# Kernel tuning notes

Measured on AMD Instinct MI355X. Metric: run time of the kernel, lower is better.

The kernel has to match this reference:

```python
import jax, jax.numpy as jnp
import numpy as np

B, C, H, W, D = 8, 64, 16, 16, 8  # D = spectral channel dim ('channle')
CQ = C // 8


def setup_inputs() -> dict:
    key = jax.random.key(0)
    ks = jax.random.split(key, 8)
    return {
        "x": jax.random.normal(ks[0], (B, C, H, W, D), dtype=jnp.float32),
        "Wq": jax.random.normal(ks[1], (CQ, C), dtype=jnp.float32) * (1.0 / np.sqrt(C)),
        "bq": jax.random.normal(ks[2], (CQ,), dtype=jnp.float32) * 0.02,
        "Wk": jax.random.normal(ks[3], (CQ, C), dtype=jnp.float32) * (1.0 / np.sqrt(C)),
        "bk": jax.random.normal(ks[4], (CQ,), dtype=jnp.float32) * 0.02,
        "Wv": jax.random.normal(ks[5], (C, C), dtype=jnp.float32) * (1.0 / np.sqrt(C)),
        "bv": jax.random.normal(ks[6], (C,), dtype=jnp.float32) * 0.02,
        "gamma": jax.random.normal(ks[7], (1,), dtype=jnp.float32),
    }


def reference(x, Wq, bq, Wk, bk, Wv, bv, gamma):
    b, c, h, w, d = x.shape
    n = h * w * d
    xf = x.reshape(b, c, n)  # flatten spatial+spectral, matches torch .view
    # 1x1x1 convs are channel-wise linear maps
    q = jnp.einsum('oc,bcn->bno', Wq, xf) + bq  # [B, N, CQ]
    k = jnp.einsum('oc,bcn->bon', Wk, xf) + bk[:, None]  # [B, CQ, N]
    energy = jnp.einsum('bno,bom->bnm', q, k)  # [B, N, N]
    attn = jax.nn.softmax(energy, axis=-1)
    v = jnp.einsum('oc,bcn->bon', Wv, xf) + bv[:, None]  # [B, C, N]
    # out[b,c,i] = sum_j v[b,c,j] * attn[b,i,j]  (bmm with attention^T)
    out = jnp.einsum('bcj,bij->bci', v, attn)
    out = out.reshape(b, c, h, w, d)
    return gamma * out + x
```

## Files before the change

### kernel.cpp

```cpp
#include <hip/hip_runtime.h>
#include <math.h>


#define NB  8
#define NC  64
#define NN  2048
#define L2E 1.44269504088896340736f
#define MST 36

typedef float f32x4 __attribute__((ext_vector_type(4)));
typedef __bf16 bf16x8 __attribute__((ext_vector_type(8)));
typedef __bf16 bf16x2 __attribute__((ext_vector_type(2)));
typedef unsigned short ushort_t;
typedef unsigned short us4 __attribute__((ext_vector_type(4)));

__device__ __forceinline__ unsigned short f2bf(float f) {
    unsigned u = __float_as_uint(f);
    u += 0x7fffu + ((u >> 16) & 1u);
    return (unsigned short)(u >> 16);
}
__device__ __forceinline__ float bf2f(unsigned short h) {
    return __uint_as_float(((unsigned)h) << 16);
}
__device__ __forceinline__ unsigned packbf(float a, float b) {
    union { bf16x2 v; unsigned u; } t;
    t.v = (bf16x2){ (__bf16)a, (__bf16)b };
    return t.u;
}

__global__ __launch_bounds__(256) void qkv_kernel(
    const float* __restrict__ x,
    const float* __restrict__ Wq, const float* __restrict__ bq,
    const float* __restrict__ Wk, const float* __restrict__ bk,
    const float* __restrict__ Wv, const float* __restrict__ bv,
    ushort_t* __restrict__ Qws, ushort_t* __restrict__ Kws,
    ushort_t* __restrict__ Vws)
{
    __shared__ float sWg[64][20];
    __shared__ float sB[16];
    __shared__ float sX[64][64];

    const int tid = threadIdx.x;
    const unsigned blk = blockIdx.x;
    const int b = blk & 7;
    const unsigned rest = blk >> 3;
    const unsigned pc = rest / 5u;
    const int og = (int)(rest - pc * 5u);
    const int n0 = (int)pc * 64;
    const int obase = og * 16;

    for (int idx = tid; idx < 1024; idx += 256) {
        const int o = idx >> 6;
        const int c = idx & 63;
        const int oo = obase + o;
        float w;
        if (oo < 8)       w = Wq[oo * NC + c] * L2E;
        else if (oo < 16) w = Wk[(oo - 8) * NC + c];
        else              w = Wv[(oo - 16) * NC + c];
        sWg[c][o] = w;
    }
    if (tid < 16) {
        const int oo = obase + tid;
        float v;
        if (oo < 8)       v = bq[oo] * L2E;
        else if (oo < 16) v = bk[oo - 8];
        else              v = bv[oo - 16];
        sB[tid] = v;
    }
    {
        const float* xg = x + (size_t)b * NC * NN + n0;
        for (int idx = tid; idx < 4096; idx += 256) {
            const int c = idx >> 6, px = idx & 63;
            sX[c][px] = xg[(size_t)c * NN + px];
        }
    }
    __syncthreads();

    const int lanepx = tid & 63;
    const int wv = tid >> 6;

    f32x4 acc = { sB[wv*4+0], sB[wv*4+1], sB[wv*4+2], sB[wv*4+3] };
    #pragma unroll
    for (int ch = 0; ch < 64; ch++) {
        const float xv = sX[ch][lanepx];
        const f32x4 w = *(const f32x4*)&sWg[ch][wv * 4];
        acc[0] = fmaf(w[0], xv, acc[0]);
        acc[1] = fmaf(w[1], xv, acc[1]);
        acc[2] = fmaf(w[2], xv, acc[2]);
        acc[3] = fmaf(w[3], xv, acc[3]);
    }

    const int n = n0 + lanepx;
    const int t  = n >> 6;

    if (og == 0) {
        us4 hi, lo;
        #pragma unroll
        for (int e = 0; e < 4; e++) {
            const unsigned short h = f2bf(acc[e]);
            hi[e] = h;
            lo[e] = f2bf(acc[e] - bf2f(h));
        }
        if (wv < 2) {
            const size_t a = (size_t)b * 32768 + (size_t)(n >> 4) * 256
                           + (size_t)(n & 15) * 8 + wv * 4;
            *(us4*)(Qws + a)       = hi;
            *(us4*)(Qws + a + 128) = lo;
        } else {
            const int jl = n & 63;
            const int fK = ((jl >> 5) & 1) + 2 * ((jl >> 2) & 1);
            const int mK = ((jl >> 3) & 3) * 4 + (jl & 3);
            const size_t a = (size_t)b * 32768 + (size_t)t * 1024
                           + (size_t)fK * 256 + (size_t)mK * 8 + (wv - 2) * 4;
            *(us4*)(Kws + a)       = hi;
            *(us4*)(Kws + a + 128) = lo;
        }
    } else {
        const int jc = (n >> 5) & 1;
        const int gg = (n >> 3) & 3;
        const int e8 = n & 7;
        const int cb = og - 1;
        const size_t base = (size_t)b * 131072 + (size_t)t * 4096
                          + (size_t)jc * 2048 + (size_t)cb * 512
                          + (size_t)gg * 8 + e8;
        #pragma unroll
        for (int e = 0; e < 4; e++)
            Vws[base + (size_t)(wv * 4 + e) * 32] = f2bf(acc[e]);
    }
}

__global__ __launch_bounds__(512, 2) void attn_kernel(
    const ushort_t* __restrict__ Qg, const ushort_t* __restrict__ Kg,
    const ushort_t* __restrict__ Vg, const float* __restrict__ x,
    const float* __restrict__ gamma, float* __restrict__ out)
{
    __shared__ __align__(16) char smem[74752];
    float* sMacc = (float*)smem;
    float* sMl   = (float*)(smem + 73728);

    const int tid  = threadIdx.x;
    const int w    = tid >> 6;
    const int rg   = w >> 2;
    const int jq   = w & 3;
    const int lane = tid & 63;
    const int li   = lane & 15;
    const int g    = lane >> 4;
    const int b    = blockIdx.x & 7;
    const int rb   = blockIdx.x >> 3;
    const int i0   = rb * 64 + rg * 32;

    const ushort_t* Kb = Kg + (size_t)b * 32768;
    const ushort_t* Vb = Vg + (size_t)b * 131072;

    const int ib0 = rb * 4 + rg * 2;
    const bf16x8 qf0 = *(const bf16x8*)(Qg + (size_t)b * 32768 + (size_t)ib0 * 256
                                        + (size_t)(g & 1) * 128 + (size_t)li * 8);
    const bf16x8 qf1 = *(const bf16x8*)(Qg + (size_t)b * 32768 + (size_t)(ib0 + 1) * 256
                                        + (size_t)(g & 1) * 128 + (size_t)li * 8);

    float l0 = 0.f, l1 = 0.f;
    f32x4 acc0[4], acc1[4];
    #pragma unroll
    for (int cb = 0; cb < 4; cb++) {
        acc0[cb] = (f32x4){0.f,0.f,0.f,0.f};
        acc1[cb] = (f32x4){0.f,0.f,0.f,0.f};
    }
    const f32x4 zero4 = {0.f,0.f,0.f,0.f};

    const ushort_t* Kp = Kb + (size_t)(jq * 8) * 1024 + (size_t)(g >> 1) * 128 + (size_t)li * 8;
    const ushort_t* Vp = Vb + (size_t)(jq * 8) * 4096 + (size_t)li * 32 + (size_t)g * 8;

    bf16x8 kc[4];
    #pragma unroll
    for (int f = 0; f < 4; f++)
        kc[f] = *(const bf16x8*)(Kp + (size_t)f * 256);

    for (int t = 0; t < 8; ++t) {
        bf16x8 vc0[4];
        #pragma unroll
        for (int cb = 0; cb < 4; cb++)
            vc0[cb] = *(const bf16x8*)(Vp + (size_t)cb * 512);

        f32x4 e[4];
        __builtin_amdgcn_s_setprio(1);
        #pragma unroll
        for (int f = 0; f < 4; f++)
            e[f] = __builtin_amdgcn_mfma_f32_16x16x32_bf16(kc[f], qf0, zero4, 0, 0, 0);
        __builtin_amdgcn_s_setprio(0);

        unsigned pkA0[4], pkB0[4];
        {
            float ls = 0.f;
            #pragma unroll
            for (int f = 0; f < 4; f++) {
                const float p0 = __builtin_amdgcn_exp2f(e[f][0]);
                const float p1 = __builtin_amdgcn_exp2f(e[f][1]);
                const float p2 = __builtin_amdgcn_exp2f(e[f][2]);
                const float p3 = __builtin_amdgcn_exp2f(e[f][3]);
                pkA0[f] = packbf(p0, p1);
                pkB0[f] = packbf(p2, p3);
                ls += (p0 + p1) + (p2 + p3);
            }
            l0 += ls;
        }

        __builtin_amdgcn_s_setprio(1);
        #pragma unroll
        for (int f = 0; f < 4; f++)
            e[f] = __builtin_amdgcn_mfma_f32_16x16x32_bf16(kc[f], qf1, zero4, 0, 0, 0);
        __builtin_amdgcn_s_setprio(0);

        if (t < 7) {
            #pragma unroll
            for (int f = 0; f < 4; f++)
                kc[f] = *(const bf16x8*)(Kp + 1024 + (size_t)f * 256);
        }
        Kp += 1024;

        unsigned pkA1[4], pkB1[4];
        {
            float ls = 0.f;
            #pragma unroll
            for (int f = 0; f < 4; f++) {
                const float p0 = __builtin_amdgcn_exp2f(e[f][0]);
                const float p1 = __builtin_amdgcn_exp2f(e[f][1]);
                const float p2 = __builtin_amdgcn_exp2f(e[f][2]);
                const float p3 = __builtin_amdgcn_exp2f(e[f][3]);
                pkA1[f] = packbf(p0, p1);
                pkB1[f] = packbf(p2, p3);
                ls += (p0 + p1) + (p2 + p3);
            }
            l1 += ls;
        }

        bf16x8 vc1[4];
        #pragma unroll
        for (int cb = 0; cb < 4; cb++)
            vc1[cb] = *(const bf16x8*)(Vp + 2048 + (size_t)cb * 512);

        __builtin_amdgcn_s_setprio(1);
        {
            union { unsigned u[4]; bf16x8 v; } pf0, pf1;
            pf0.u[0] = pkA0[0]; pf0.u[1] = pkB0[0]; pf0.u[2] = pkA0[2]; pf0.u[3] = pkB0[2];
            pf1.u[0] = pkA1[0]; pf1.u[1] = pkB1[0]; pf1.u[2] = pkA1[2]; pf1.u[3] = pkB1[2];
            #pragma unroll
            for (int cb = 0; cb < 4; cb++) {
                acc0[cb] = __builtin_amdgcn_mfma_f32_16x16x32_bf16(vc0[cb], pf0.v, acc0[cb], 0, 0, 0);
                acc1[cb] = __builtin_amdgcn_mfma_f32_16x16x32_bf16(vc0[cb], pf1.v, acc1[cb], 0, 0, 0);
            }
        }
        {
            union { unsigned u[4]; bf16x8 v; } pf0, pf1;
            pf0.u[0] = pkA0[1]; pf0.u[1] = pkB0[1]; pf0.u[2] = pkA0[3]; pf0.u[3] = pkB0[3];
            pf1.u[0] = pkA1[1]; pf1.u[1] = pkB1[1]; pf1.u[2] = pkA1[3]; pf1.u[3] = pkB1[3];
            #pragma unroll
            for (int cb = 0; cb < 4; cb++) {
                acc0[cb] = __builtin_amdgcn_mfma_f32_16x16x32_bf16(vc1[cb], pf0.v, acc0[cb], 0, 0, 0);
                acc1[cb] = __builtin_amdgcn_mfma_f32_16x16x32_bf16(vc1[cb], pf1.v, acc1[cb], 0, 0, 0);
            }
        }
        __builtin_amdgcn_s_setprio(0);
        Vp += 4096;
    }

    l0 += __shfl_xor(l0, 16); l0 += __shfl_xor(l0, 32);
    l1 += __shfl_xor(l1, 16); l1 += __shfl_xor(l1, 32);

    __syncthreads();
    {
        float* ap = sMacc + (size_t)(w * 64 + lane) * MST;
        #pragma unroll
        for (int cb = 0; cb < 4; cb++) {
            *(f32x4*)(ap + cb * 4)      = acc0[cb];
            *(f32x4*)(ap + 16 + cb * 4) = acc1[cb];
        }
        if (g == 0) {
            sMl[w * 32 + li]      = l0;
            sMl[w * 32 + 16 + li] = l1;
        }
    }
    __syncthreads();

    {
        const int r = lane & 31;
        const float gmv = gamma[0];
        #pragma unroll
        for (int u = 0; u < 2; u++) {
            const int cq   = jq * 4 + (lane >> 5) * 2 + u;
            const int g_s  = cq & 3;
            const int cb_s = cq >> 2;
            const int ib_s = r >> 4;
            const int li_s = r & 15;
            const int srcln = g_s * 16 + li_s;
            const int aidx  = ib_s * 16 + cb_s * 4;

            float L = 0.f;
            float num0 = 0.f, num1 = 0.f, num2 = 0.f, num3 = 0.f;
            #pragma unroll
            for (int q = 0; q < 4; q++) {
                const int w2 = rg * 4 + q;
                L += sMl[w2 * 32 + r];
                const f32x4 a = *(const f32x4*)(sMacc + (size_t)(w2 * 64 + srcln) * MST + aidx);
                num0 += a[0]; num1 += a[1]; num2 += a[2]; num3 += a[3];
            }
            const float inv = 1.0f / L;
            const size_t gb = (size_t)b * NC * NN + i0 + r;
            const size_t c0 = (size_t)cq * 4;
            out[gb + (c0 + 0) * NN] = fmaf(gmv, num0 * inv, x[gb + (c0 + 0) * NN]);
            out[gb + (c0 + 1) * NN] = fmaf(gmv, num1 * inv, x[gb + (c0 + 1) * NN]);
            out[gb + (c0 + 2) * NN] = fmaf(gmv, num2 * inv, x[gb + (c0 + 2) * NN]);
            out[gb + (c0 + 3) * NN] = fmaf(gmv, num3 * inv, x[gb + (c0 + 3) * NN]);
        }
    }
}

extern "C" void kernel_launch(void* const* d_in, const int* in_sizes, int n_in,
                              void* d_out, int out_size, void* d_ws, size_t ws_size,
                              hipStream_t stream) {
    const float* x     = (const float*)d_in[0];
    const float* Wq    = (const float*)d_in[1];
    const float* bq    = (const float*)d_in[2];
    const float* Wk    = (const float*)d_in[3];
    const float* bk    = (const float*)d_in[4];
    const float* Wv    = (const float*)d_in[5];
    const float* bv    = (const float*)d_in[6];
    const float* gamma = (const float*)d_in[7];
    float* out = (float*)d_out;

    ushort_t* Qws = (ushort_t*)d_ws;
    ushort_t* Kws = Qws + (size_t)NB * 32768;
    ushort_t* Vws = Kws + (size_t)NB * 32768;

    qkv_kernel<<<1280, 256, 0, stream>>>(x, Wq, bq, Wk, bk, Wv, bv, Qws, Kws, Vws);
    attn_kernel<<<NB * 32, 512, 0, stream>>>(Qws, Kws, Vws, x, gamma, out);
}
```

Measured before the change: 24.20 us.

## Software-pipeline attention loop so PV MFMAs overlap next QK and exp

Restructures the inner loop into a software pipeline. A prologue computes the first tile's scores and probabilities. Each later iteration issues the next QK MFMAs together with the PV MFMAs of the previous tile, prefetches V one full tile ahead, and then runs the exp/pack work, with an epilogue finishing the last PV. The aim is to hide exp latency and global V load latency behind MFMA work, at the cost of more live registers (double-buffered V, 16 packed probability words) and a fully unrolled loop, which may hurt occupancy.

```diff
diff --git a/kernel.cpp b/kernel.cpp
--- a/kernel.cpp
+++ b/kernel.cpp
@@ -167,100 +167,136 @@
     }
     const f32x4 zero4 = {0.f,0.f,0.f,0.f};
 
-    const ushort_t* Kp = Kb + (size_t)(jq * 8) * 1024 + (size_t)(g >> 1) * 128 + (size_t)li * 8;
-    const ushort_t* Vp = Vb + (size_t)(jq * 8) * 4096 + (size_t)li * 32 + (size_t)g * 8;
-
-    bf16x8 kc[4];
-    #pragma unroll
-    for (int f = 0; f < 4; f++)
-        kc[f] = *(const bf16x8*)(Kp + (size_t)f * 256);
-
-    for (int t = 0; t < 8; ++t) {
-        bf16x8 vc0[4];
-        #pragma unroll
-        for (int cb = 0; cb < 4; cb++)
-            vc0[cb] = *(const bf16x8*)(Vp + (size_t)cb * 512);
-
-        f32x4 e[4];
+    const ushort_t* Kq = Kb + (size_t)(jq * 8) * 1024 + (size_t)(g >> 1) * 128 + (size_t)li * 8;
+    const ushort_t* Vq = Vb + (size_t)(jq * 8) * 4096 + (size_t)li * 32 + (size_t)g * 8;
+
+    bf16x8 kc[4], vcA[8];
+    unsigned pkP[16];
+
+    #pragma unroll
+    for (int f = 0; f < 4; f++) kc[f] = *(const bf16x8*)(Kq + (size_t)f * 256);
+    #pragma unroll
+    for (int u = 0; u < 8; u++)
+        vcA[u] = *(const bf16x8*)(Vq + (size_t)(u >> 2) * 2048 + (size_t)(u & 3) * 512);
+
+    {
+        f32x4 e0[4], e1[4];
         __builtin_amdgcn_s_setprio(1);
         #pragma unroll
         for (int f = 0; f < 4; f++)
-            e[f] = __builtin_amdgcn_mfma_f32_16x16x32_bf16(kc[f], qf0, zero4, 0, 0, 0);
+            e0[f] = __builtin_amdgcn_mfma_f32_16x16x32_bf16(kc[f], qf0, zero4, 0, 0, 0);
+        #pragma unroll
+        for (int f = 0; f < 4; f++)
+            e1[f] = __builtin_amdgcn_mfma_f32_16x16x32_bf16(kc[f], qf1, zero4, 0, 0, 0);
         __builtin_amdgcn_s_setprio(0);
-
-        unsigned pkA0[4], pkB0[4];
+        #pragma unroll
+        for (int f = 0; f < 4; f++)
+            kc[f] = *(const bf16x8*)(Kq + 1024 + (size_t)f * 256);
+        float ls0 = 0.f, ls1 = 0.f;
+        #pragma unroll
+        for (int f = 0; f < 4; f++) {
+            const float a0 = __builtin_amdgcn_exp2f(e0[f][0]);
+            const float a1 = __builtin_amdgcn_exp2f(e0[f][1]);
+            const float a2 = __builtin_amdgcn_exp2f(e0[f][2]);
+            const float a3 = __builtin_amdgcn_exp2f(e0[f][3]);
+            pkP[f]     = packbf(a0, a1);
+            pkP[4 + f] = packbf(a2, a3);
+            ls0 += (a0 + a1) + (a2 + a3);
+            const float c0 = __builtin_amdgcn_exp2f(e1[f][0]);
+            const float c1 = __builtin_amdgcn_exp2f(e1[f][1]);
+            const float c2 = __builtin_amdgcn_exp2f(e1[f][2]);
+            const float c3 = __builtin_amdgcn_exp2f(e1[f][3]);
+            pkP[8 + f]  = packbf(c0, c1);
+            pkP[12 + f] = packbf(c2, c3);
+            ls1 += (c0 + c1) + (c2 + c3);
+        }
+        l0 += ls0; l1 += ls1;
+    }
+
+    #pragma unroll
+    for (int t = 0; t < 7; ++t) {
+        bf16x8 vcB[8];
+        #pragma unroll
+        for (int u = 0; u < 8; u++)
+            vcB[u] = *(const bf16x8*)(Vq + (size_t)(t + 1) * 4096
+                                      + (size_t)(u >> 2) * 2048 + (size_t)(u & 3) * 512);
+
+        f32x4 e0[4], e1[4];
+        __builtin_amdgcn_s_setprio(1);
+        #pragma unroll
+        for (int f = 0; f < 4; f++)
+            e0[f] = __builtin_amdgcn_mfma_f32_16x16x32_bf16(kc[f], qf0, zero4, 0, 0, 0);
+        #pragma unroll
+        for (int f = 0; f < 4; f++)
+            e1[f] = __builtin_amdgcn_mfma_f32_16x16x32_bf16(kc[f], qf1, zero4, 0, 0, 0);
+
         {
-            float ls = 0.f;
+            union { unsigned u[4]; bf16x8 v; } pf0, pf1;
+            pf0.u[0] = pkP[0]; pf0.u[1] = pkP[4]; pf0.u[2] = pkP[2]; pf0.u[3] = pkP[6];
+            pf1.u[0] = pkP[8]; pf1.u[1] = pkP[12]; pf1.u[2] = pkP[10]; pf1.u[3] = pkP[14];
             #pragma unroll
-            for (int f = 0; f < 4; f++) {
-                const float p0 = __builtin_amdgcn_exp2f(e[f][0]);
-                const float p1 = __builtin_amdgcn_exp2f(e[f][1]);
-                const float p2 = __builtin_amdgcn_exp2f(e[f][2]);
-                const float p3 = __builtin_amdgcn_exp2f(e[f][3]);
-                pkA0[f] = packbf(p0, p1);
-                pkB0[f] = packbf(p2, p3);
-                ls += (p0 + p1) + (p2 + p3);
+            for (int cb = 0; cb < 4; cb++) {
+                acc0[cb] = __builtin_amdgcn_mfma_f32_16x16x32_bf16(vcA[cb], pf0.v, acc0[cb], 0, 0, 0);
+                acc1[cb] = __builtin_amdgcn_mfma_f32_16x16x32_bf16(vcA[cb], pf1.v, acc1[cb], 0, 0, 0);
             }
-            l0 += ls;
-        }
-
-        __builtin_amdgcn_s_setprio(1);
-        #pragma unroll
-        for (int f = 0; f < 4; f++)
-            e[f] = __builtin_amdgcn_mfma_f32_16x16x32_bf16(kc[f], qf1, zero4, 0, 0, 0);
+            pf0.u[0] = pkP[1]; pf0.u[1] = pkP[5]; pf0.u[2] = pkP[3]; pf0.u[3] = pkP[7];
+            pf1.u[0] = pkP[9]; pf1.u[1] = pkP[13]; pf1.u[2] = pkP[11]; pf1.u[3] = pkP[15];
+            #pragma unroll
+            for (int cb = 0; cb < 4; cb++) {
+                acc0[cb] = __builtin_amdgcn_mfma_f32_16x16x32_bf16(vcA[4 + cb], pf0.v, acc0[cb], 0, 0, 0);
+                acc1[cb] = __builtin_amdgcn_mfma_f32_16x16x32_bf16(vcA[4 + cb], pf1.v, acc1[cb], 0, 0, 0);
+            }
+        }
         __builtin_amdgcn_s_setprio(0);
 
-        if (t < 7) {
+        if (t < 6) {
             #pragma unroll
             for (int f = 0; f < 4; f++)
-                kc[f] = *(const bf16x8*)(Kp + 1024 + (size_t)f * 256);
-        }
-        Kp += 1024;
-
-        unsigned pkA1[4], pkB1[4];
-        {
-            float ls = 0.f;
-            #pragma unroll
-            for (int f = 0; f < 4; f++) {
-                const float p0 = __builtin_amdgcn_exp2f(e[f][0]);
-                const float p1 = __builtin_amdgcn_exp2f(e[f][1]);
-                const float p2 = __builtin_amdgcn_exp2f(e[f][2]);
-                const float p3 = __builtin_amdgcn_exp2f(e[f][3]);
-                pkA1[f] = packbf(p0, p1);
-                pkB1[f] = packbf(p2, p3);
-                ls += (p0 + p1) + (p2 + p3);
-            }
-            l1 += ls;
-        }
-
-        bf16x8 vc1[4];
-        #pragma unroll
-        for (int cb = 0; cb < 4; cb++)
-            vc1[cb] = *(const bf16x8*)(Vp + 2048 + (size_t)cb * 512);
-
+                kc[f] = *(const bf16x8*)(Kq + (size_t)(t + 2) * 1024 + (size_t)f * 256);
+        }
+
+        float ls0 = 0.f, ls1 = 0.f;
+        #pragma unroll
+        for (int f = 0; f < 4; f++) {
+            const float a0 = __builtin_amdgcn_exp2f(e0[f][0]);
+            const float a1 = __builtin_amdgcn_exp2f(e0[f][1]);
+            const float a2 = __builtin_amdgcn_exp2f(e0[f][2]);
+            const float a3 = __builtin_amdgcn_exp2f(e0[f][3]);
+            pkP[f]     = packbf(a0, a1);
+            pkP[4 + f] = packbf(a2, a3);
+            ls0 += (a0 + a1) + (a2 + a3);
+            const float c0 = __builtin_amdgcn_exp2f(e1[f][0]);
+            const float c1 = __builtin_amdgcn_exp2f(e1[f][1]);
+            const float c2 = __builtin_amdgcn_exp2f(e1[f][2]);
+            const float c3 = __builtin_amdgcn_exp2f(e1[f][3]);
+            pkP[8 + f]  = packbf(c0, c1);
+            pkP[12 + f] = packbf(c2, c3);
+            ls1 += (c0 + c1) + (c2 + c3);
+        }
+        l0 += ls0; l1 += ls1;
+
+        #pragma unroll
+        for (int u = 0; u < 8; u++) vcA[u] = vcB[u];
+    }
+
+    {
+        union { unsigned u[4]; bf16x8 v; } pf0, pf1;
         __builtin_amdgcn_s_setprio(1);
-        {
-            union { unsigned u[4]; bf16x8 v; } pf0, pf1;
-            pf0.u[0] = pkA0[0]; pf0.u[1] = pkB0[0]; pf0.u[2] = pkA0[2]; pf0.u[3] = pkB0[2];
-            pf1.u[0] = pkA1[0]; pf1.u[1] = pkB1[0]; pf1.u[2] = pkA1[2]; pf1.u[3] = pkB1[2];
-            #pragma unroll
-            for (int cb = 0; cb < 4; cb++) {
-                acc0[cb] = __builtin_amdgcn_mfma_f32_16x16x32_bf16(vc0[cb], pf0.v, acc0[cb], 0, 0, 0);
-                acc1[cb] = __builtin_amdgcn_mfma_f32_16x16x32_bf16(vc0[cb], pf1.v, acc1[cb], 0, 0, 0);
-            }
-        }
-        {
-            union { unsigned u[4]; bf16x8 v; } pf0, pf1;
-            pf0.u[0] = pkA0[1]; pf0.u[1] = pkB0[1]; pf0.u[2] = pkA0[3]; pf0.u[3] = pkB0[3];
-            pf1.u[0] = pkA1[1]; pf1.u[1] = pkB1[1]; pf1.u[2] = pkA1[3]; pf1.u[3] = pkB1[3];
-            #pragma unroll
-            for (int cb = 0; cb < 4; cb++) {
-                acc0[cb] = __builtin_amdgcn_mfma_f32_16x16x32_bf16(vc1[cb], pf0.v, acc0[cb], 0, 0, 0);
-                acc1[cb] = __builtin_amdgcn_mfma_f32_16x16x32_bf16(vc1[cb], pf1.v, acc1[cb], 0, 0, 0);
-            }
+        pf0.u[0] = pkP[0]; pf0.u[1] = pkP[4]; pf0.u[2] = pkP[2]; pf0.u[3] = pkP[6];
+        pf1.u[0] = pkP[8]; pf1.u[1] = pkP[12]; pf1.u[2] = pkP[10]; pf1.u[3] = pkP[14];
+        #pragma unroll
+        for (int cb = 0; cb < 4; cb++) {
+            acc0[cb] = __builtin_amdgcn_mfma_f32_16x16x32_bf16(vcA[cb], pf0.v, acc0[cb], 0, 0, 0);
+            acc1[cb] = __builtin_amdgcn_mfma_f32_16x16x32_bf16(vcA[cb], pf1.v, acc1[cb], 0, 0, 0);
+        }
+        pf0.u[0] = pkP[1]; pf0.u[1] = pkP[5]; pf0.u[2] = pkP[3]; pf0.u[3] = pkP[7];
+        pf1.u[0] = pkP[9]; pf1.u[1] = pkP[13]; pf1.u[2] = pkP[11]; pf1.u[3] = pkP[15];
+        #pragma unroll
+        for (int cb = 0; cb < 4; cb++) {
+            acc0[cb] = __builtin_amdgcn_mfma_f32_16x16x32_bf16(vcA[4 + cb], pf0.v, acc0[cb], 0, 0, 0);
+            acc1[cb] = __builtin_amdgcn_mfma_f32_16x16x32_bf16(vcA[4 + cb], pf1.v, acc1[cb], 0, 0, 0);
         }
         __builtin_amdgcn_s_setprio(0);
-        Vp += 4096;
     }
 
     l0 += __shfl_xor(l0, 16); l0 += __shfl_xor(l0, 32);
```

After: 24.45 us. Within noise of the previous version (+1.0%).

## Fuse QKV projection and attention into one kernel with a grid-wide flag barrier

Applied to the files above, without the earlier changes.

Merges the QKV projection kernel and the attention kernel into a single persistent launch of 256 blocks. Each block first projects its 64-pixel tile to all 80 output channels and writes Q/K/V to the workspace. A global atomic counter, reset by a memset before the launch, then acts as a grid barrier before the attention phase. This removes one kernel launch and the gap between the two kernels. In exchange the projection now runs on only 256 blocks instead of 1280, and correctness relies on all 256 blocks being resident at once.

```diff
diff --git a/kernel.cpp b/kernel.cpp
--- a/kernel.cpp
+++ b/kernel.cpp
@@ -7,6 +7,7 @@
 #define NN  2048
 #define L2E 1.44269504088896340736f
 #define MST 36
+#define FLAG_OFF 3145728
 
 typedef float f32x4 __attribute__((ext_vector_type(4)));
 typedef __bf16 bf16x8 __attribute__((ext_vector_type(8)));
@@ -28,288 +29,317 @@
     return t.u;
 }
 
-__global__ __launch_bounds__(256) void qkv_kernel(
+__global__ __launch_bounds__(512, 2) void pam_fused(
     const float* __restrict__ x,
     const float* __restrict__ Wq, const float* __restrict__ bq,
     const float* __restrict__ Wk, const float* __restrict__ bk,
     const float* __restrict__ Wv, const float* __restrict__ bv,
+    const float* __restrict__ gamma,
     ushort_t* __restrict__ Qws, ushort_t* __restrict__ Kws,
-    ushort_t* __restrict__ Vws)
+    ushort_t* __restrict__ Vws, unsigned* __restrict__ flag,
+    float* __restrict__ out)
 {
-    __shared__ float sWg[64][20];
-    __shared__ float sB[16];
-    __shared__ float sX[64][64];
+    __shared__ __align__(16) char smem[74752];
 
     const int tid = threadIdx.x;
-    const unsigned blk = blockIdx.x;
-    const int b = blk & 7;
-    const unsigned rest = blk >> 3;
-    const unsigned pc = rest / 5u;
-    const int og = (int)(rest - pc * 5u);
-    const int n0 = (int)pc * 64;
-    const int obase = og * 16;
-
-    for (int idx = tid; idx < 1024; idx += 256) {
-        const int o = idx >> 6;
-        const int c = idx & 63;
-        const int oo = obase + o;
-        float w;
-        if (oo < 8)       w = Wq[oo * NC + c] * L2E;
-        else if (oo < 16) w = Wk[(oo - 8) * NC + c];
-        else              w = Wv[(oo - 16) * NC + c];
-        sWg[c][o] = w;
+    const int b  = blockIdx.x & 7;
+    const int rb = blockIdx.x >> 3;
+
+    {
+        float* sW = (float*)smem;
+        float* sX = (float*)smem + 6400;
+        float* sB = (float*)smem + 6400 + 4352;
+
+        for (int idx = tid; idx < 5120; idx += 512) {
+            const int o = idx >> 6, c = idx & 63;
+            float w;
+            if (o < 8)       w = Wq[o * NC + c] * L2E;
+            else if (o < 16) w = Wk[(o - 8) * NC + c];
+            else             w = Wv[(o - 16) * NC + c];
+            sW[c * 100 + (o / 10) * 12 + (o % 10)] = w;
+        }
+        if (tid < 80) {
+            const int o = tid;
+            float v;
+            if (o < 8)       v = bq[o] * L2E;
+            else if (o < 16) v = bk[o - 8];
+            else             v = bv[o - 16];
+            sB[(o / 10) * 12 + (o % 10)] = v;
+        }
+        {
+            const float* xg = x + (size_t)b * NC * NN + rb * 64;
+            for (int idx = tid; idx < 4096; idx += 512) {
+                const int c = idx >> 6, px = idx & 63;
+                sX[c * 68 + px] = xg[(size_t)c * NN + px];
+            }
+        }
+        __syncthreads();
+
+        const int px = tid & 63;
+        const int sg = tid >> 6;
+        const int n  = rb * 64 + px;
+
+        f32x4 a0 = *(const f32x4*)(sB + sg * 12);
+        f32x4 a1 = *(const f32x4*)(sB + sg * 12 + 4);
+        f32x4 a2 = *(const f32x4*)(sB + sg * 12 + 8);
+        const float* wrow = sW + sg * 12;
+        #pragma unroll
+        for (int ch = 0; ch < 64; ch++) {
+            const float xv = sX[ch * 68 + px];
+            const f32x4 w0 = *(const f32x4*)(wrow + ch * 100);
+            const f32x4 w1 = *(const f32x4*)(wrow + ch * 100 + 4);
+            const f32x4 w2 = *(const f32x4*)(wrow + ch * 100 + 8);
+            a0[0] = fmaf(w0[0], xv, a0[0]); a0[1] = fmaf(w0[1], xv, a0[1]);
+            a0[2] = fmaf(w0[2], xv, a0[2]); a0[3] = fmaf(w0[3], xv, a0[3]);
+            a1[0] = fmaf(w1[0], xv, a1[0]); a1[1] = fmaf(w1[1], xv, a1[1]);
+            a1[2] = fmaf(w1[2], xv, a1[2]); a1[3] = fmaf(w1[3], xv, a1[3]);
+            a2[0] = fmaf(w2[0], xv, a2[0]); a2[1] = fmaf(w2[1], xv, a2[1]);
+            a2[2] = fmaf(w2[2], xv, a2[2]); a2[3] = fmaf(w2[3], xv, a2[3]);
+        }
+
+        float av[10];
+        av[0]=a0[0]; av[1]=a0[1]; av[2]=a0[2]; av[3]=a0[3];
+        av[4]=a1[0]; av[5]=a1[1]; av[6]=a1[2]; av[7]=a1[3];
+        av[8]=a2[0]; av[9]=a2[1];
+
+        const int jl = px;
+        const int fK = ((jl >> 5) & 1) + 2 * ((jl >> 2) & 1);
+        const int mK = ((jl >> 3) & 3) * 4 + (jl & 3);
+        const size_t kbase = (size_t)b * 32768 + (size_t)rb * 1024
+                           + (size_t)fK * 256 + (size_t)mK * 8;
+        const int jc = (px >> 5) & 1;
+        const int gg = (px >> 3) & 3;
+        const int e8 = px & 7;
+        const size_t vbase = (size_t)b * 131072 + (size_t)rb * 4096
+                           + (size_t)jc * 2048 + (size_t)gg * 8 + e8;
+
+        if (sg == 0) {
+            us4 h0, h1, l0v, l1v;
+            #pragma unroll
+            for (int e = 0; e < 4; e++) {
+                const unsigned short h = f2bf(av[e]);
+                h0[e] = h; l0v[e] = f2bf(av[e] - bf2f(h));
+            }
+            #pragma unroll
+            for (int e = 0; e < 4; e++) {
+                const unsigned short h = f2bf(av[4 + e]);
+                h1[e] = h; l1v[e] = f2bf(av[4 + e] - bf2f(h));
+            }
+            const size_t qa = (size_t)b * 32768 + (size_t)(n >> 4) * 256
+                            + (size_t)(n & 15) * 8;
+            *(us4*)(Qws + qa)       = h0; *(us4*)(Qws + qa + 4)       = h1;
+            *(us4*)(Qws + qa + 128) = l0v; *(us4*)(Qws + qa + 132)    = l1v;
+            #pragma unroll
+            for (int u = 8; u < 10; u++) {
+                const unsigned short h = f2bf(av[u]);
+                Kws[kbase + (u - 8)]       = h;
+                Kws[kbase + (u - 8) + 128] = f2bf(av[u] - bf2f(h));
+            }
+        } else if (sg == 1) {
+            #pragma unroll
+            for (int u = 0; u < 6; u++) {
+                const unsigned short h = f2bf(av[u]);
+                Kws[kbase + 2 + u]       = h;
+                Kws[kbase + 2 + u + 128] = f2bf(av[u] - bf2f(h));
+            }
+            #pragma unroll
+            for (int u = 6; u < 10; u++) {
+                const int c = u - 6;
+                Vws[vbase + (size_t)(c >> 4) * 512 + (size_t)(c & 15) * 32] = f2bf(av[u]);
+            }
+        } else {
+            #pragma unroll
+            for (int u = 0; u < 10; u++) {
+                const int c = sg * 10 - 16 + u;
+                Vws[vbase + (size_t)(c >> 4) * 512 + (size_t)(c & 15) * 32] = f2bf(av[u]);
+            }
+        }
     }
-    if (tid < 16) {
-        const int oo = obase + tid;
-        float v;
-        if (oo < 8)       v = bq[oo] * L2E;
-        else if (oo < 16) v = bk[oo - 8];
-        else              v = bv[oo - 16];
-        sB[tid] = v;
-    }
-    {
-        const float* xg = x + (size_t)b * NC * NN + n0;
-        for (int idx = tid; idx < 4096; idx += 256) {
-            const int c = idx >> 6, px = idx & 63;
-            sX[c][px] = xg[(size_t)c * NN + px];
-        }
+
+    __syncthreads();
+    __threadfence();
+    if (tid == 0) {
+        __hip_atomic_fetch_add(flag, 1u, __ATOMIC_ACQ_REL, __HIP_MEMORY_SCOPE_AGENT);
+        while (__hip_atomic_load(flag, __ATOMIC_ACQUIRE, __HIP_MEMORY_SCOPE_AGENT) < 256u)
+            __builtin_amdgcn_s_sleep(8);
     }
     __syncthreads();
-
-    const int lanepx = tid & 63;
-    const int wv = tid >> 6;
-
-    f32x4 acc = { sB[wv*4+0], sB[wv*4+1], sB[wv*4+2], sB[wv*4+3] };
-    #pragma unroll
-    for (int ch = 0; ch < 64; ch++) {
-        const float xv = sX[ch][lanepx];
-        const f32x4 w = *(const f32x4*)&sWg[ch][wv * 4];
-        acc[0] = fmaf(w[0], xv, acc[0]);
-        acc[1] = fmaf(w[1], xv, acc[1]);
-        acc[2] = fmaf(w[2], xv, acc[2]);
-        acc[3] = fmaf(w[3], xv, acc[3]);
-    }
-
-    const int n = n0 + lanepx;
-    const int t  = n >> 6;
-
-    if (og == 0) {
-        us4 hi, lo;
+    __threadfence();
+
+    {
+        float* sMacc = (float*)smem;
+        float* sMl   = (float*)(smem + 73728);
+
+        const int w    = tid >> 6;
+        const int rg   = w >> 2;
+        const int jq   = w & 3;
+        const int lane = tid & 63;
+        const int li   = lane & 15;
+        const int g    = lane >> 4;
+        const int i0   = rb * 64 + rg * 32;
+
+        const ushort_t* Kb = Kws + (size_t)b * 32768;
+        const ushort_t* Vb = Vws + (size_t)b * 131072;
+
+        const int ib0 = rb * 4 + rg * 2;
+        const bf16x8 qf0 = *(const bf16x8*)(Qws + (size_t)b * 32768 + (size_t)ib0 * 256
+                                            + (size_t)(g & 1) * 128 + (size_t)li * 8);
+        const bf16x8 qf1 = *(const bf16x8*)(Qws + (size_t)b * 32768 + (size_t)(ib0 + 1) * 256
+                                            + (size_t)(g & 1) * 128 + (size_t)li * 8);
+
+        float l0 = 0.f, l1 = 0.f;
+        f32x4 acc0[4], acc1[4];
         #pragma unroll
-        for (int e = 0; e < 4; e++) {
-            const unsigned short h = f2bf(acc[e]);
-            hi[e] = h;
-            lo[e] = f2bf(acc[e] - bf2f(h));
-        }
-        if (wv < 2) {
-            const size_t a = (size_t)b * 32768 + (size_t)(n >> 4) * 256
-                           + (size_t)(n & 15) * 8 + wv * 4;
-            *(us4*)(Qws + a)       = hi;
-            *(us4*)(Qws + a + 128) = lo;
-        } else {
-            const int jl = n & 63;
-            const int fK = ((jl >> 5) & 1) + 2 * ((jl >> 2) & 1);
-            const int mK = ((jl >> 3) & 3) * 4 + (jl & 3);
-            const size_t a = (size_t)b * 32768 + (size_t)t * 1024
-                           + (size_t)fK * 256 + (size_t)mK * 8 + (wv - 2) * 4;
-            *(us4*)(Kws + a)       = hi;
-            *(us4*)(Kws + a + 128) = lo;
-        }
-    } else {
-        const int jc = (n >> 5) & 1;
-        const int gg = (n >> 3) & 3;
-        const int e8 = n & 7;
-        const int cb = og - 1;
-        const size_t base = (size_t)b * 131072 + (size_t)t * 4096
-                          + (size_t)jc * 2048 + (size_t)cb * 512
-                          + (size_t)gg * 8 + e8;
-        #pragma unroll
-        for (int e = 0; e < 4; e++)
-            Vws[base + (size_t)(wv * 4 + e) * 32] = f2bf(acc[e]);
-    }
-}
-
-__global__ __launch_bounds__(512, 2) void attn_kernel(
-    const ushort_t* __restrict__ Qg, const ushort_t* __restrict__ Kg,
-    const ushort_t* __restrict__ Vg, const float* __restrict__ x,
-    const float* __restrict__ gamma, float* __restrict__ out)
-{
-    __shared__ __align__(16) char smem[74752];
-    float* sMacc = (float*)smem;
-    float* sMl   = (float*)(smem + 73728);
-
-    const int tid  = threadIdx.x;
-    const int w    = tid >> 6;
-    const int rg   = w >> 2;
-    const int jq   = w & 3;
-    const int lane = tid & 63;
-    const int li   = lane & 15;
-    const int g    = lane >> 4;
-    const int b    = blockIdx.x & 7;
-    const int rb   = blockIdx.x >> 3;
-    const int i0   = rb * 64 + rg * 32;
-
-    const ushort_t* Kb = Kg + (size_t)b * 32768;
-    const ushort_t* Vb = Vg + (size_t)b * 131072;
-
-    const int ib0 = rb * 4 + rg * 2;
-    const bf16x8 qf0 = *(const bf16x8*)(Qg + (size_t)b * 32768 + (size_t)ib0 * 256
-                                        + (size_t)(g & 1) * 128 + (size_t)li * 8);
-    const bf16x8 qf1 = *(const bf16x8*)(Qg + (size_t)b * 32768 + (size_t)(ib0 + 1) * 256
-                                        + (size_t)(g & 1) * 128 + (size_t)li * 8);
-
-    float l0 = 0.f, l1 = 0.f;
-    f32x4 acc0[4], acc1[4];
-    #pragma unroll
-    for (int cb = 0; cb < 4; cb++) {
-        acc0[cb] = (f32x4){0.f,0.f,0.f,0.f};
-        acc1[cb] = (f32x4){0.f,0.f,0.f,0.f};
-    }
-    const f32x4 zero4 = {0.f,0.f,0.f,0.f};
-
-    const ushort_t* Kp = Kb + (size_t)(jq * 8) * 1024 + (size_t)(g >> 1) * 128 + (size_t)li * 8;
-    const ushort_t* Vp = Vb + (size_t)(jq * 8) * 4096 + (size_t)li * 32 + (size_t)g * 8;
-
-    bf16x8 kc[4];
-    #pragma unroll
-    for (int f = 0; f < 4; f++)
-        kc[f] = *(const bf16x8*)(Kp + (size_t)f * 256);
-
-    for (int t = 0; t < 8; ++t) {
-        bf16x8 vc0[4];
-        #pragma unroll
-        for (int cb = 0; cb < 4; cb++)
-            vc0[cb] = *(const bf16x8*)(Vp + (size_t)cb * 512);
-
-        f32x4 e[4];
-        __builtin_amdgcn_s_setprio(1);
+        for (int cb = 0; cb < 4; cb++) {
+            acc0[cb] = (f32x4){0.f,0.f,0.f,0.f};
+            acc1[cb] = (f32x4){0.f,0.f,0.f,0.f};
+        }
+        const f32x4 zero4 = {0.f,0.f,0.f,0.f};
+
+        const ushort_t* Kp = Kb + (size_t)(jq * 8) * 1024 + (size_t)(g >> 1) * 128 + (size_t)li * 8;
+        const ushort_t* Vp = Vb + (size_t)(jq * 8) * 4096 + (size_t)li * 32 + (size_t)g * 8;
+
+        bf16x8 kc[4];
         #pragma unroll
         for (int f = 0; f < 4; f++)
-            e[f] = __builtin_amdgcn_mfma_f32_16x16x32_bf16(kc[f], qf0, zero4, 0, 0, 0);
-        __builtin_amdgcn_s_setprio(0);
-
-        unsigned pkA0[4], pkB0[4];
+            kc[f] = *(const bf16x8*)(Kp + (size_t)f * 256);
+
+        for (int t = 0; t < 8; ++t) {
+            bf16x8 vc0[4];
+            #pragma unroll
+            for (int cb = 0; cb < 4; cb++)
+                vc0[cb] = *(const bf16x8*)(Vp + (size_t)cb * 512);
+
+            f32x4 e[4];
+            __builtin_amdgcn_s_setprio(1);
+            #pragma unroll
+            for (int f = 0; f < 4; f++)
+                e[f] = __builtin_amdgcn_mfma_f32_16x16x32_bf16(kc[f], qf0, zero4, 0, 0, 0);
+            __builtin_amdgcn_s_setprio(0);
+
+            unsigned pkA0[4], pkB0[4];
+            {
+                float ls = 0.f;
+                #pragma unroll
+                for (int f = 0; f < 4; f++) {
+                    const float p0 = __builtin_amdgcn_exp2f(e[f][0]);
+                    const float p1 = __builtin_amdgcn_exp2f(e[f][1]);
+                    const float p2 = __builtin_amdgcn_exp2f(e[f][2]);
+                    const float p3 = __builtin_amdgcn_exp2f(e[f][3]);
+                    pkA0[f] = packbf(p0, p1);
+                    pkB0[f] = packbf(p2, p3);
+                    ls += (p0 + p1) + (p2 + p3);
+                }
+                l0 += ls;
+            }
+
+            __builtin_amdgcn_s_setprio(1);
+            #pragma unroll
+            for (int f = 0; f < 4; f++)
+                e[f] = __builtin_amdgcn_mfma_f32_16x16x32_bf16(kc[f], qf1, zero4, 0, 0, 0);
+            __builtin_amdgcn_s_setprio(0);
+
+            if (t < 7) {
+                #pragma unroll
+                for (int f = 0; f < 4; f++)
+                    kc[f] = *(const bf16x8*)(Kp + 1024 + (size_t)f * 256);
+            }
+            Kp += 1024;
+
+            unsigned pkA1[4], pkB1[4];
+            {
+                float ls = 0.f;
+                #pragma unroll
+                for (int f = 0; f < 4; f++) {
+                    const float p0 = __builtin_amdgcn_exp2f(e[f][0]);
+                    const float p1 = __builtin_amdgcn_exp2f(e[f][1]);
+                    const float p2 = __builtin_amdgcn_exp2f(e[f][2]);
+                    const float p3 = __builtin_amdgcn_exp2f(e[f][3]);
+                    pkA1[f] = packbf(p0, p1);
+                    pkB1[f] = packbf(p2, p3);
+                    ls += (p0 + p1) + (p2 + p3);
+                }
+                l1 += ls;
+            }
+
+            bf16x8 vc1[4];
+            #pragma unroll
+            for (int cb = 0; cb < 4; cb++)
+                vc1[cb] = *(const bf16x8*)(Vp + 2048 + (size_t)cb * 512);
+
+            __builtin_amdgcn_s_setprio(1);
+            {
+                union { unsigned u[4]; bf16x8 v; } pf0, pf1;
+                pf0.u[0] = pkA0[0]; pf0.u[1] = pkB0[0]; pf0.u[2] = pkA0[2]; pf0.u[3] = pkB0[2];
+                pf1.u[0] = pkA1[0]; pf1.u[1] = pkB1[0]; pf1.u[2] = pkA1[2]; pf1.u[3] = pkB1[2];
+                #pragma unroll
+                for (int cb = 0; cb < 4; cb++) {
+                    acc0[cb] = __builtin_amdgcn_mfma_f32_16x16x32_bf16(vc0[cb], pf0.v, acc0[cb], 0, 0, 0);
+                    acc1[cb] = __builtin_amdgcn_mfma_f32_16x16x32_bf16(vc0[cb], pf1.v, acc1[cb], 0, 0, 0);
+                }
+            }
+            {
+                union { unsigned u[4]; bf16x8 v; } pf0, pf1;
+                pf0.u[0] = pkA0[1]; pf0.u[1] = pkB0[1]; pf0.u[2] = pkA0[3]; pf0.u[3] = pkB0[3];
+                pf1.u[0] = pkA1[1]; pf1.u[1] = pkB1[1]; pf1.u[2] = pkA1[3]; pf1.u[3] = pkB1[3];
+                #pragma unroll
+                for (int cb = 0; cb < 4; cb++) {
+                    acc0[cb] = __builtin_amdgcn_mfma_f32_16x16x32_bf16(vc1[cb], pf0.v, acc0[cb], 0, 0, 0);
+                    acc1[cb] = __builtin_amdgcn_mfma_f32_16x16x32_bf16(vc1[cb], pf1.v, acc1[cb], 0, 0, 0);
+                }
+            }
+            __builtin_amdgcn_s_setprio(0);
+            Vp += 4096;
+        }
+
+        l0 += __shfl_xor(l0, 16); l0 += __shfl_xor(l0, 32);
+        l1 += __shfl_xor(l1, 16); l1 += __shfl_xor(l1, 32);
+
+        __syncthreads();
         {
-            float ls = 0.f;
-            #pragma unroll
-            for (int f = 0; f < 4; f++) {
-                const float p0 = __builtin_amdgcn_exp2f(e[f][0]);
-                const float p1 = __builtin_amdgcn_exp2f(e[f][1]);
-                const float p2 = __builtin_amdgcn_exp2f(e[f][2]);
-                const float p3 = __builtin_amdgcn_exp2f(e[f][3]);
-                pkA0[f] = packbf(p0, p1);
-                pkB0[f] = packbf(p2, p3);
-                ls += (p0 + p1) + (p2 + p3);
-            }
-            l0 += ls;
-        }
-
-        __builtin_amdgcn_s_setprio(1);
-        #pragma unroll
-        for (int f = 0; f < 4; f++)
-            e[f] = __builtin_amdgcn_mfma_f32_16x16x32_bf16(kc[f], qf1, zero4, 0, 0, 0);
-        __builtin_amdgcn_s_setprio(0);
-
-        if (t < 7) {
-            #pragma unroll
-            for (int f = 0; f < 4; f++)
-                kc[f] = *(const bf16x8*)(Kp + 1024 + (size_t)f * 256);
-        }
-        Kp += 1024;
-
-        unsigned pkA1[4], pkB1[4];
+            float* ap = sMacc + (size_t)(w * 64 + lane) * MST;
+            #pragma unroll
+            for (int cb = 0; cb < 4; cb++) {
+                *(f32x4*)(ap + cb * 4)      = acc0[cb];
+                *(f32x4*)(ap + 16 + cb * 4) = acc1[cb];
+            }
+            if (g == 0) {
+                sMl[w * 32 + li]      = l0;
+                sMl[w * 32 + 16 + li] = l1;
+            }
+        }
+        __syncthreads();
+
         {
-            float ls = 0.f;
-            #pragma unroll
-            for (int f = 0; f < 4; f++) {
-                const float p0 = __builtin_amdgcn_exp2f(e[f][0]);
-                const float p1 = __builtin_amdgcn_exp2f(e[f][1]);
-                const float p2 = __builtin_amdgcn_exp2f(e[f][2]);
-                const float p3 = __builtin_amdgcn_exp2f(e[f][3]);
-                pkA1[f] = packbf(p0, p1);
-                pkB1[f] = packbf(p2, p3);
-                ls += (p0 + p1) + (p2 + p3);
-            }
-            l1 += ls;
-        }
-
-        bf16x8 vc1[4];
-        #pragma unroll
-        for (int cb = 0; cb < 4; cb++)
-            vc1[cb] = *(const bf16x8*)(Vp + 2048 + (size_t)cb * 512);
-
-        __builtin_amdgcn_s_setprio(1);
-        {
-            union { unsigned u[4]; bf16x8 v; } pf0, pf1;
-            pf0.u[0] = pkA0[0]; pf0.u[1] = pkB0[0]; pf0.u[2] = pkA0[2]; pf0.u[3] = pkB0[2];
-            pf1.u[0] = pkA1[0]; pf1.u[1] = pkB1[0]; pf1.u[2] = pkA1[2]; pf1.u[3] = pkB1[2];
-            #pragma unroll
-            for (int cb = 0; cb < 4; cb++) {
-                acc0[cb] = __builtin_amdgcn_mfma_f32_16x16x32_bf16(vc0[cb], pf0.v, acc0[cb], 0, 0, 0);
-                acc1[cb] = __builtin_amdgcn_mfma_f32_16x16x32_bf16(vc0[cb], pf1.v, acc1[cb], 0, 0, 0);
-            }
-        }
-        {
-            union { unsigned u[4]; bf16x8 v; } pf0, pf1;
-            pf0.u[0] = pkA0[1]; pf0.u[1] = pkB0[1]; pf0.u[2] = pkA0[3]; pf0.u[3] = pkB0[3];
-            pf1.u[0] = pkA1[1]; pf1.u[1] = pkB1[1]; pf1.u[2] = pkA1[3]; pf1.u[3] = pkB1[3];
-            #pragma unroll
-            for (int cb = 0; cb < 4; cb++) {
-                acc0[cb] = __builtin_amdgcn_mfma_f32_16x16x32_bf16(vc1[cb], pf0.v, acc0[cb], 0, 0, 0);
-                acc1[cb] = __builtin_amdgcn_mfma_f32_16x16x32_bf16(vc1[cb], pf1.v, acc1[cb], 0, 0, 0);
-            }
-        }
-        __builtin_amdgcn_s_setprio(0);
-        Vp += 4096;
-    }
-
-    l0 += __shfl_xor(l0, 16); l0 += __shfl_xor(l0, 32);
-    l1 += __shfl_xor(l1, 16); l1 += __shfl_xor(l1, 32);
-
-    __syncthreads();
-    {
-        float* ap = sMacc + (size_t)(w * 64 + lane) * MST;
-        #pragma unroll
-        for (int cb = 0; cb < 4; cb++) {
-            *(f32x4*)(ap + cb * 4)      = acc0[cb];
-            *(f32x4*)(ap + 16 + cb * 4) = acc1[cb];
-        }
-        if (g == 0) {
-            sMl[w * 32 + li]      = l0;
-            sMl[w * 32 + 16 + li] = l1;
-        }
-    }
-    __syncthreads();
-
-    {
-        const int r = lane & 31;
-        const float gmv = gamma[0];
-        #pragma unroll
-        for (int u = 0; u < 2; u++) {
-            const int cq   = jq * 4 + (lane >> 5) * 2 + u;
-            const int g_s  = cq & 3;
-            const int cb_s = cq >> 2;
-            const int ib_s = r >> 4;
-            const int li_s = r & 15;
-            const int srcln = g_s * 16 + li_s;
-            const int aidx  = ib_s * 16 + cb_s * 4;
-
-            float L = 0.f;
-            float num0 = 0.f, num1 = 0.f, num2 = 0.f, num3 = 0.f;
-            #pragma unroll
-            for (int q = 0; q < 4; q++) {
-                const int w2 = rg * 4 + q;
-                L += sMl[w2 * 32 + r];
-                const f32x4 a = *(const f32x4*)(sMacc + (size_t)(w2 * 64 + srcln) * MST + aidx);
-                num0 += a[0]; num1 += a[1]; num2 += a[2]; num3 += a[3];
-            }
-            const float inv = 1.0f / L;
-            const size_t gb = (size_t)b * NC * NN + i0 + r;
-            const size_t c0 = (size_t)cq * 4;
-            out[gb + (c0 + 0) * NN] = fmaf(gmv, num0 * inv, x[gb + (c0 + 0) * NN]);
-            out[gb + (c0 + 1) * NN] = fmaf(gmv, num1 * inv, x[gb + (c0 + 1) * NN]);
-            out[gb + (c0 + 2) * NN] = fmaf(gmv, num2 * inv, x[gb + (c0 + 2) * NN]);
-            out[gb + (c0 + 3) * NN] = fmaf(gmv, num3 * inv, x[gb + (c0 + 3) * NN]);
+            const int r = lane & 31;
+            const float gmv = gamma[0];
+            #pragma unroll
+            for (int u = 0; u < 2; u++) {
+                const int cq   = jq * 4 + (lane >> 5) * 2 + u;
+                const int g_s  = cq & 3;
+                const int cb_s = cq >> 2;
+                const int ib_s = r >> 4;
+                const int li_s = r & 15;
+                const int srcln = g_s * 16 + li_s;
+                const int aidx  = ib_s * 16 + cb_s * 4;
+
+                float L = 0.f;
+                float num0 = 0.f, num1 = 0.f, num2 = 0.f, num3 = 0.f;
+                #pragma unroll
+                for (int q = 0; q < 4; q++) {
+                    const int w2 = rg * 4 + q;
+                    L += sMl[w2 * 32 + r];
+                    const f32x4 a = *(const f32x4*)(sMacc + (size_t)(w2 * 64 + srcln) * MST + aidx);
+                    num0 += a[0]; num1 += a[1]; num2 += a[2]; num3 += a[3];
+                }
+                const float inv = 1.0f / L;
+                const size_t gb = (size_t)b * NC * NN + i0 + r;
+                const size_t c0 = (size_t)cq * 4;
+                out[gb + (c0 + 0) * NN] = fmaf(gmv, num0 * inv, x[gb + (c0 + 0) * NN]);
+                out[gb + (c0 + 1) * NN] = fmaf(gmv, num1 * inv, x[gb + (c0 + 1) * NN]);
+                out[gb + (c0 + 2) * NN] = fmaf(gmv, num2 * inv, x[gb + (c0 + 2) * NN]);
+                out[gb + (c0 + 3) * NN] = fmaf(gmv, num3 * inv, x[gb + (c0 + 3) * NN]);
+            }
         }
     }
 }
@@ -330,7 +360,9 @@
     ushort_t* Qws = (ushort_t*)d_ws;
     ushort_t* Kws = Qws + (size_t)NB * 32768;
     ushort_t* Vws = Kws + (size_t)NB * 32768;
-
-    qkv_kernel<<<1280, 256, 0, stream>>>(x, Wq, bq, Wk, bk, Wv, bv, Qws, Kws, Vws);
-    attn_kernel<<<NB * 32, 512, 0, stream>>>(Qws, Kws, Vws, x, gamma, out);
-}
+    unsigned* flag = (unsigned*)((char*)d_ws + FLAG_OFF);
+
+    hipMemsetAsync(flag, 0, 4, stream);
+    pam_fused<<<256, 512, 0, stream>>>(x, Wq, bq, Wk, bk, Wv, bv, gamma,
+                                       Qws, Kws, Vws, flag, out);
+}
```

Result: slower. 95.92 us (+296.3%).
